# Performance work log

Hardware: AMD Instinct MI355X
Metric: run time of the kernel (lower is better)

Reference implementation:

```python
import jax, jax.numpy as jnp
import numpy as np

DIM = 1024
NUM_HEADS = 16
HEAD_DIM = DIM // NUM_HEADS
EPS = 1e-6


def setup_inputs() -> dict:
    key = jax.random.key(0)
    ks = jax.random.split(key, 9)
    B, S = 4, 4096
    std = 1.0 / np.sqrt(DIM)
    inp = {
        "x": jax.random.normal(ks[0], (B, S, DIM), dtype=jnp.float32),
        "attention_mask": jnp.ones((B, S), dtype=jnp.float32),
        "Wq": jax.random.normal(ks[1], (DIM, DIM), dtype=jnp.float32) * std,
        "bq": jnp.zeros((DIM,), dtype=jnp.float32),
        "Wk": jax.random.normal(ks[2], (DIM, DIM), dtype=jnp.float32) * std,
        "bk": jnp.zeros((DIM,), dtype=jnp.float32),
        "Wv": jax.random.normal(ks[3], (DIM, DIM), dtype=jnp.float32) * std,
        "bv": jnp.zeros((DIM,), dtype=jnp.float32),
        "Wo": jax.random.normal(ks[4], (DIM, DIM), dtype=jnp.float32) * std,
        "bo": jnp.zeros((DIM,), dtype=jnp.float32),
    }
    return inp


def _phi(x):
    # ELU + 1 feature map (positive-valued kernel features)
    return jax.nn.elu(x) + 1.0


def reference(x, attention_mask, Wq, bq, Wk, bk, Wv, bv, Wo, bo):
    B, S, _ = x.shape
    H, D = NUM_HEADS, HEAD_DIM
    q = (x @ Wq.T + bq).reshape(B, S, H, D)
    k = (x @ Wk.T + bk).reshape(B, S, H, D)
    v = (x @ Wv.T + bv).reshape(B, S, H, D)
    q = _phi(q)
    k = _phi(k)
    m = attention_mask[:, :, None, None]
    k = k * m
    v = v * m
    # kv state: [B, H, D, D]
    kv = jnp.einsum("bshd,bshm->bhdm", k, v)
    qkv = jnp.einsum("bshd,bhdm->bshm", q, kv)
    k_sum = k.sum(axis=1)  # [B, H, D]
    normalizer = jnp.einsum("bshd,bhd->bsh", q, k_sum) + EPS
    out = (qkv / normalizer[..., None]).reshape(B, S, DIM)
    return out @ Wo.T + bo
```

## Files before the change

kernel.cpp:

```cpp
#include <hip/hip_runtime.h>

typedef unsigned short u16;
typedef float f32x4 __attribute__((ext_vector_type(4)));
typedef __bf16 bf16x8 __attribute__((ext_vector_type(8)));
typedef unsigned short us8 __attribute__((ext_vector_type(8)));
typedef __attribute__((address_space(3))) const char* lds3_t;

#define EPS_ 1e-6f

__device__ __forceinline__ u16 f2bf(float f) {
    unsigned u = __float_as_uint(f);
    u += 0x7FFFu + ((u >> 16) & 1u);
    return (u16)(u >> 16);
}
__device__ __forceinline__ float bf2f(u16 h) {
    return __uint_as_float(((unsigned)h) << 16);
}
__device__ __forceinline__ void gload_lds16(const void* g, void* l) {
    __builtin_amdgcn_global_load_lds(
        (const __attribute__((address_space(1))) void*)g,
        (__attribute__((address_space(3))) void*)l, 16, 0, 0);
}

__global__ __launch_bounds__(256) void f32_to_bf16_kernel(
    const float* __restrict__ src, u16* __restrict__ dst, int n4)
{
    int i = blockIdx.x * 256 + threadIdx.x;
    if (i >= n4) return;
    float4 f = ((const float4*)src)[i];
    ushort4 o;
    o.x = f2bf(f.x); o.y = f2bf(f.y); o.z = f2bf(f.z); o.w = f2bf(f.w);
    ((ushort4*)dst)[i] = o;
}

__global__ __launch_bounds__(256) void w_convert_fused(
    const float* __restrict__ Wq, const float* __restrict__ Wk,
    const float* __restrict__ Wv, const float* __restrict__ bq,
    const float* __restrict__ bk, const float* __restrict__ bv,
    u16* __restrict__ wqkvbf, float* __restrict__ bcat)
{
    int b = blockIdx.x;
    if (b < 3072) {
        const float* src = (b < 1024) ? Wq : ((b < 2048) ? Wk : Wv);
        int which = b >> 10, lb = b & 1023;
        int i = lb * 256 + threadIdx.x;
        float4 f = ((const float4*)src)[i];
        ushort4 o;
        o.x = f2bf(f.x); o.y = f2bf(f.y); o.z = f2bf(f.z); o.w = f2bf(f.w);
        ((ushort4*)(wqkvbf + (size_t)which * 1048576))[i] = o;
    } else {
        int which = b - 3072;
        const float* src = (which == 0) ? bq : ((which == 1) ? bk : bv);
        ((float4*)(bcat + which * 1024))[threadIdx.x] =
            ((const float4*)src)[threadIdx.x];
    }
}


__device__ __forceinline__ void stage_half(
    const u16* __restrict__ src, int K, int kbase, char* slot, int tid)
{
    const int w = tid >> 6, l = tid & 63;
    #pragma unroll
    for (int j = 0; j < 2; ++j) {
        int c16 = j * 512 + w * 64 + l;
        int row = c16 >> 2;
        int sl  = c16 & 3;
        int ksrc = kbase + ((sl ^ ((row >> 1) & 3)) << 3);
        gload_lds16(src + (size_t)row * K + ksrc, slot + j * 8192 + w * 1024);
    }
}

#define BARRIER()  asm volatile("s_barrier" ::: "memory")
#define VMCNT4()   asm volatile("s_waitcnt vmcnt(4)" ::: "memory")
#define VMCNT0()   asm volatile("s_waitcnt vmcnt(0)" ::: "memory")

#define DSR_(dst_, base_, OFFSTR_) \
    asm volatile("ds_read_b128 %0, %1 offset:" OFFSTR_ \
                 : "=v"(dst_) : "v"((lds3_t)(base_)))
#define DSR(dst_, base_, OFF_) DSR_(dst_, base_, #OFF_)

#define LGKM_(NSTR_) asm volatile("s_waitcnt lgkmcnt(" NSTR_ ")" ::: "memory")
#define LGKM(N_) do { LGKM_(#N_); __builtin_amdgcn_sched_barrier(0); } while (0)

#define MFMA1(M_, N_, AF_, BF_) \
    acc[M_][N_] = __builtin_amdgcn_mfma_f32_16x16x32_bf16(BF_, AF_, acc[M_][N_], 0, 0, 0)

#define QUAD(M0, A0_, A1_, A2_, A3_, B0_, B1_, B2_, B3_) do { \
    __builtin_amdgcn_s_setprio(1); \
    MFMA1(M0+0, 0, A0_, B0_); MFMA1(M0+0, 1, A0_, B1_); MFMA1(M0+0, 2, A0_, B2_); MFMA1(M0+0, 3, A0_, B3_); \
    MFMA1(M0+1, 0, A1_, B0_); MFMA1(M0+1, 1, A1_, B1_); MFMA1(M0+1, 2, A1_, B2_); MFMA1(M0+1, 3, A1_, B3_); \
    MFMA1(M0+2, 0, A2_, B0_); MFMA1(M0+2, 1, A2_, B1_); MFMA1(M0+2, 2, A2_, B2_); MFMA1(M0+2, 3, A2_, B3_); \
    MFMA1(M0+3, 0, A3_, B0_); MFMA1(M0+3, 1, A3_, B1_); MFMA1(M0+3, 2, A3_, B2_); MFMA1(M0+3, 3, A3_, B3_); \
    __builtin_amdgcn_s_setprio(0); \
} while (0)

template<int MODE>
__global__ __launch_bounds__(512, 2) void gemm8p(
    const u16* __restrict__ A, const u16* __restrict__ B,
    const float* __restrict__ bias,
    u16* __restrict__ oq, u16* __restrict__ ok, u16* __restrict__ ov,
    float* __restrict__ outf, int M, int N, int K)
{
    extern __shared__ char lds[];
    const int tid  = threadIdx.x;
    const int lane = tid & 63;
    const int wv   = tid >> 6;
    const int wm   = wv >> 2;
    const int wn   = wv & 3;
    const int NT = K >> 6;

    int bx, by;
    {
        const int gx = gridDim.x;
        int wg  = blockIdx.y * gx + blockIdx.x;
        int cpx = (gx * gridDim.y) >> 3;
        int swz = (wg & 7) * cpx + (wg >> 3);
        bx = swz % gx; by = swz / gx;
    }

    const u16* Ab = A + (size_t)by * 256 * K;
    const u16* Bb = B + (size_t)bx * 256 * K;

    const int i  = lane & 15, g = lane >> 4;
    const int fo = ((g ^ ((i >> 1) & 3)) << 4);
    const int aoff = (wm * 128 + i) * 64 + fo;
    const int boff = (wn * 64 + i) * 64 + fo;

    f32x4 acc[8][4];
    #pragma unroll
    for (int m = 0; m < 8; ++m)
        #pragma unroll
        for (int n = 0; n < 4; ++n) {
            acc[m][n][0] = 0.f; acc[m][n][1] = 0.f;
            acc[m][n][2] = 0.f; acc[m][n][3] = 0.f;
        }

    stage_half(Ab, K, 0,  lds + 0,             tid);
    stage_half(Bb, K, 0,  lds + 16384,         tid);
    stage_half(Ab, K, 32, lds + 32768,         tid);
    stage_half(Bb, K, 32, lds + 49152,         tid);
    stage_half(Ab, K, 64, lds + 65536 + 0,     tid);
    stage_half(Bb, K, 64, lds + 65536 + 16384, tid);

    for (int t = 0; t < NT; ++t) {
        char* cb = lds + ((t & 1) << 16);
        char* nb = lds + (((t + 1) & 1) << 16);
        const int t1 = (t + 1 < NT) ? t + 1 : NT - 1;
        const int t2 = (t + 2 < NT) ? t + 2 : NT - 1;

        VMCNT4();
        BARRIER();

        const char* aK0 = cb + aoff;
        const char* bK0 = cb + 16384 + boff;
        const char* aK1 = cb + 32768 + aoff;
        const char* bK1 = cb + 49152 + boff;

        bf16x8 aL0, aL1, aL2, aL3, aH0, aH1, aH2, aH3, b00, b01, b02, b03;
        bf16x8 cL0, cL1, cL2, cL3, cH0, cH1, cH2, cH3, b10, b11, b12, b13;

        DSR(b00, bK0, 0); DSR(b01, bK0, 1024); DSR(b02, bK0, 2048); DSR(b03, bK0, 3072);
        DSR(aL0, aK0, 0); DSR(aL1, aK0, 1024); DSR(aL2, aK0, 2048); DSR(aL3, aK0, 3072);
        DSR(aH0, aK0, 4096); DSR(aH1, aK0, 5120); DSR(aH2, aK0, 6144); DSR(aH3, aK0, 7168);

        stage_half(Ab, K, t1 * 64 + 32, nb + 32768, tid);
        stage_half(Bb, K, t1 * 64 + 32, nb + 49152, tid);

        LGKM(4);
        QUAD(0, aL0, aL1, aL2, aL3, b00, b01, b02, b03);

        DSR(b10, bK1, 0); DSR(b11, bK1, 1024); DSR(b12, bK1, 2048); DSR(b13, bK1, 3072);
        DSR(cL0, aK1, 0); DSR(cL1, aK1, 1024); DSR(cL2, aK1, 2048); DSR(cL3, aK1, 3072);
        DSR(cH0, aK1, 4096); DSR(cH1, aK1, 5120); DSR(cH2, aK1, 6144); DSR(cH3, aK1, 7168);

        LGKM(12);
        QUAD(4, aH0, aH1, aH2, aH3, b00, b01, b02, b03);

        BARRIER();
        stage_half(Ab, K, t2 * 64, cb + 0,     tid);
        stage_half(Bb, K, t2 * 64, cb + 16384, tid);

        LGKM(4);
        QUAD(0, cL0, cL1, cL2, cL3, b10, b11, b12, b13);
        LGKM(0);
        QUAD(4, cH0, cH1, cH2, cH3, b10, b11, b12, b13);
    }
    VMCNT0();

    const int rowg0 = by * 256 + wm * 128;
    const int colg0 = bx * 256 + wn * 64;

    if (MODE == 1) {
        const int which = colg0 >> 10;
        u16* dst = (which == 0) ? oq : ((which == 1) ? ok : ov);
        const bool dophi = (which < 2);
        const int cbo = colg0 & 1023;
        float4 bs[4];
        #pragma unroll
        for (int n = 0; n < 4; ++n)
            bs[n] = *(const float4*)(bias + colg0 + n * 16 + g * 4);
        #pragma unroll
        for (int m = 0; m < 8; ++m) {
            int row = rowg0 + m * 16 + i;
            #pragma unroll
            for (int n = 0; n < 4; ++n) {
                float v0 = acc[m][n][0] + bs[n].x;
                float v1 = acc[m][n][1] + bs[n].y;
                float v2 = acc[m][n][2] + bs[n].z;
                float v3 = acc[m][n][3] + bs[n].w;
                if (dophi) {
                    v0 = (v0 > 0.f) ? (v0 + 1.f) : __expf(v0);
                    v1 = (v1 > 0.f) ? (v1 + 1.f) : __expf(v1);
                    v2 = (v2 > 0.f) ? (v2 + 1.f) : __expf(v2);
                    v3 = (v3 > 0.f) ? (v3 + 1.f) : __expf(v3);
                }
                ushort4 o;
                o.x = f2bf(v0); o.y = f2bf(v1); o.z = f2bf(v2); o.w = f2bf(v3);
                *(ushort4*)(dst + (size_t)row * 1024 + cbo + n * 16 + g * 4) = o;
            }
        }
    } else {
        float4 bs[4];
        #pragma unroll
        for (int n = 0; n < 4; ++n)
            bs[n] = *(const float4*)(bias + colg0 + n * 16 + g * 4);
        #pragma unroll
        for (int m = 0; m < 8; ++m) {
            int row = rowg0 + m * 16 + i;
            #pragma unroll
            for (int n = 0; n < 4; ++n) {
                float4 o;
                o.x = acc[m][n][0] + bs[n].x;
                o.y = acc[m][n][1] + bs[n].y;
                o.z = acc[m][n][2] + bs[n].z;
                o.w = acc[m][n][3] + bs[n].w;
                *(float4*)(outf + (size_t)row * N + colg0 + n * 16 + g * 4) = o;
            }
        }
    }
}

__global__ __launch_bounds__(256) void kv_partial(
    const u16* __restrict__ kbf, const u16* __restrict__ vbf,
    const float* __restrict__ mask, float* __restrict__ kvp, float* __restrict__ ksp)
{
    const int bh = blockIdx.x, ch = blockIdx.y;
    const int b = bh >> 4, h = bh & 15;
    const int tid = threadIdx.x;
    __shared__ __align__(16) float ks[32][64];
    __shared__ __align__(16) float vs[32][64];
    const int dg = tid >> 4, mg = tid & 15;
    float acc[4][4] = {};
    float ksa[4] = {};
    const int s0 = ch * 256;
    const int lr = tid >> 3, lc = (tid & 7) * 8;
    for (int sb = 0; sb < 256; sb += 32) {
        {
            size_t grow = (size_t)b * 4096 + (s0 + sb + lr);
            float mm = mask[grow];
            size_t off = (grow << 10) + (h << 6) + lc;
            us8 ku = __builtin_bit_cast(us8, *(const bf16x8*)(kbf + off));
            us8 vu = __builtin_bit_cast(us8, *(const bf16x8*)(vbf + off));
            float4 k0, k1, v0, v1;
            k0.x = bf2f(ku[0]) * mm; k0.y = bf2f(ku[1]) * mm;
            k0.z = bf2f(ku[2]) * mm; k0.w = bf2f(ku[3]) * mm;
            k1.x = bf2f(ku[4]) * mm; k1.y = bf2f(ku[5]) * mm;
            k1.z = bf2f(ku[6]) * mm; k1.w = bf2f(ku[7]) * mm;
            v0.x = bf2f(vu[0]) * mm; v0.y = bf2f(vu[1]) * mm;
            v0.z = bf2f(vu[2]) * mm; v0.w = bf2f(vu[3]) * mm;
            v1.x = bf2f(vu[4]) * mm; v1.y = bf2f(vu[5]) * mm;
            v1.z = bf2f(vu[6]) * mm; v1.w = bf2f(vu[7]) * mm;
            *(float4*)&ks[lr][lc]     = k0;
            *(float4*)&ks[lr][lc + 4] = k1;
            *(float4*)&vs[lr][lc]     = v0;
            *(float4*)&vs[lr][lc + 4] = v1;
        }
        __syncthreads();
        #pragma unroll
        for (int ss = 0; ss < 32; ++ss) {
            float4 k4 = *(const float4*)&ks[ss][dg << 2];
            float4 v4 = *(const float4*)&vs[ss][mg << 2];
            float ka[4] = {k4.x, k4.y, k4.z, k4.w};
            float va[4] = {v4.x, v4.y, v4.z, v4.w};
            #pragma unroll
            for (int di = 0; di < 4; ++di) {
                ksa[di] += ka[di];
                #pragma unroll
                for (int mi = 0; mi < 4; ++mi) acc[di][mi] += ka[di] * va[mi];
            }
        }
        __syncthreads();
    }
    float* o = kvp + (((size_t)ch * 64 + bh) << 12);
    #pragma unroll
    for (int di = 0; di < 4; ++di)
        #pragma unroll
        for (int mi = 0; mi < 4; ++mi)
            o[(dg * 4 + di) * 64 + (mg * 4 + mi)] = acc[di][mi];
    if (mg == 0) {
        float* os = ksp + (((size_t)ch * 64 + bh) << 6);
        #pragma unroll
        for (int di = 0; di < 4; ++di) os[dg * 4 + di] = ksa[di];
    }
}

__global__ __launch_bounds__(256) void kv_reduce(
    const float* __restrict__ kvp, const float* __restrict__ ksp,
    u16* __restrict__ kvTbf, u16* __restrict__ ksumbf)
{
    const int bh = blockIdx.x, tid = threadIdx.x;
    for (int idx = tid; idx < 4096; idx += 256) {
        float s = 0.f;
        #pragma unroll
        for (int c = 0; c < 16; ++c) s += kvp[(((size_t)c * 64 + bh) << 12) + idx];
        int d = idx >> 6, m = idx & 63;
        kvTbf[((size_t)bh << 12) + (m << 6) + d] = f2bf(s);
    }
    if (tid < 64) {
        float s = 0.f;
        #pragma unroll
        for (int c = 0; c < 16; ++c) s += ksp[(((size_t)c * 64 + bh) << 6) + tid];
        ksumbf[(bh << 6) + tid] = f2bf(s);
    }
}

__global__ __launch_bounds__(256) void attn_kernel(
    const u16* __restrict__ qbf, const u16* __restrict__ kvTbf,
    const u16* __restrict__ ksumbf, u16* __restrict__ attnbf)
{
    const int bh = blockIdx.x;
    const int b = bh >> 4, h = bh & 15;
    const int tid = threadIdx.x, lane = tid & 63, wv = tid >> 6;
    __shared__ __align__(16) u16 kvs[64 * 64];
    __shared__ __align__(16) u16 kss[64];

    {
        const uint4* src = (const uint4*)(kvTbf + ((size_t)bh << 12));
        for (int u = tid; u < 512; u += 256) {
            uint4 d4 = src[u];
            int m = u >> 3, slot = u & 7;
            *(uint4*)((char*)kvs + m * 128 + ((slot ^ (m & 7)) << 4)) = d4;
        }
        if (tid < 32)
            ((unsigned*)kss)[tid] = ((const unsigned*)(ksumbf + ((size_t)bh << 6)))[tid];
    }
    __syncthreads();

    bf16x8 bfr[2][4], bnf[2];
    #pragma unroll
    for (int kk = 0; kk < 2; ++kk) {
        int kslot = kk * 4 + (lane >> 4);
        #pragma unroll
        for (int n = 0; n < 4; ++n) {
            int m = n * 16 + (lane & 15);
            bfr[kk][n] = *(const bf16x8*)((const char*)kvs + m * 128 +
                                          ((kslot ^ (m & 7)) << 4));
        }
        #pragma unroll
        for (int i2 = 0; i2 < 8; ++i2) bnf[kk][i2] = (__bf16)0.0f;
        if ((lane & 15) == 0)
            bnf[kk] = *(const bf16x8*)((const char*)kss + (kslot << 4));
    }

    const int sbase = blockIdx.y * 256 + wv * 16;
    for (int it = 0; it < 4; ++it) {
        const int st = sbase + it * 64;
        f32x4 acc[4], nacc;
        #pragma unroll
        for (int n = 0; n < 4; ++n) {
            acc[n][0] = 0.f; acc[n][1] = 0.f; acc[n][2] = 0.f; acc[n][3] = 0.f;
        }
        nacc[0] = 0.f; nacc[1] = 0.f; nacc[2] = 0.f; nacc[3] = 0.f;
        #pragma unroll
        for (int kk = 0; kk < 2; ++kk) {
            size_t goff = (((size_t)(b * 4096 + st + (lane & 15))) << 10) +
                          (h << 6) + kk * 32 + ((lane >> 4) << 3);
            bf16x8 af = *(const bf16x8*)(qbf + goff);
            #pragma unroll
            for (int n = 0; n < 4; ++n)
                acc[n] = __builtin_amdgcn_mfma_f32_16x16x32_bf16(af, bfr[kk][n], acc[n], 0, 0, 0);
            nacc = __builtin_amdgcn_mfma_f32_16x16x32_bf16(af, bnf[kk], nacc, 0, 0, 0);
        }
        float inv[4];
        #pragma unroll
        for (int j = 0; j < 4; ++j) {
            float nj = __shfl(nacc[j], lane & 48);
            inv[j] = 1.0f / (nj + EPS_);
        }
        #pragma unroll
        for (int n = 0; n < 4; ++n)
            #pragma unroll
            for (int j = 0; j < 4; ++j) {
                int row = st + ((lane >> 4) << 2) + j;
                attnbf[(((size_t)(b * 4096 + row)) << 10) + (h << 6) + n * 16 + (lane & 15)]
                    = f2bf(acc[n][j] * inv[j]);
            }
    }
}

extern "C" void kernel_launch(void* const* d_in, const int* in_sizes, int n_in,
                              void* d_out, int out_size, void* d_ws, size_t ws_size,
                              hipStream_t stream) {
    const float* x    = (const float*)d_in[0];
    const float* mask = (const float*)d_in[1];
    const float* Wq   = (const float*)d_in[2];
    const float* bq   = (const float*)d_in[3];
    const float* Wk   = (const float*)d_in[4];
    const float* bk   = (const float*)d_in[5];
    const float* Wv   = (const float*)d_in[6];
    const float* bv   = (const float*)d_in[7];
    const float* Wo   = (const float*)d_in[8];
    const float* bo   = (const float*)d_in[9];
    float* out = (float*)d_out;

    if (ws_size < 142606336u) return;

    char* ws = (char*)d_ws;
    u16*   xbf    = (u16*)ws;
    u16*   wqkvbf = (u16*)(ws + 33554432);
    float* bcat   = (float*)(ws + 39845888);
    u16*   qbf    = (u16*)(ws + 41943040);
    u16*   kbf    = qbf + 16777216;
    u16*   vbf    = kbf + 16777216;
    u16*   attnbf = kbf;
    float* kvp    = (float*)ws;
    float* ksp    = (float*)(ws + 16777216);
    u16*   kvTbf  = (u16*)(ws + 17039360);
    u16*   ksumbf = (u16*)(ws + 17563648);
    u16*   wobf   = (u16*)(ws + 20971520);

    f32_to_bf16_kernel<<<16384, 256, 0, stream>>>(x, xbf, 16777216 / 4);
    w_convert_fused<<<3075, 256, 0, stream>>>(Wq, Wk, Wv, bq, bk, bv, wqkvbf, bcat);

    gemm8p<1><<<dim3(12, 64), 512, 131072, stream>>>(
        xbf, wqkvbf, bcat, qbf, kbf, vbf, nullptr, 16384, 3072, 1024);

    f32_to_bf16_kernel<<<1024, 256, 0, stream>>>(Wo, wobf, 1048576 / 4);

    kv_partial<<<dim3(64, 16), 256, 0, stream>>>(kbf, vbf, mask, kvp, ksp);
    kv_reduce<<<64, 256, 0, stream>>>(kvp, ksp, kvTbf, ksumbf);

    attn_kernel<<<dim3(64, 16), 256, 0, stream>>>(qbf, kvTbf, ksumbf, attnbf);

    gemm8p<0><<<dim3(4, 64), 512, 131072, stream>>>(
        attnbf, wobf, bo, nullptr, nullptr, nullptr, out, 16384, 1024, 1024);
}
```

Baseline: 225.4 us.

## Shrink GEMM block tile to 256x128 with 4 waves and triple-buffered K32 pipeline

```diff
diff --git a/kernel.cpp b/kernel.cpp
--- a/kernel.cpp
+++ b/kernel.cpp
@@ -57,22 +57,35 @@
 }
 
 
-__device__ __forceinline__ void stage_half(
+__device__ __forceinline__ void stage_a(
+    const u16* __restrict__ src, int K, int kbase, char* slot, int tid)
+{
+    const int w = tid >> 6, l = tid & 63;
+    #pragma unroll
+    for (int j = 0; j < 4; ++j) {
+        int c16 = j * 256 + w * 64 + l;
+        int row = c16 >> 2;
+        int sl  = c16 & 3;
+        int ksrc = kbase + ((sl ^ ((row >> 1) & 3)) << 3);
+        gload_lds16(src + (size_t)row * K + ksrc, slot + j * 4096 + w * 1024);
+    }
+}
+__device__ __forceinline__ void stage_b(
     const u16* __restrict__ src, int K, int kbase, char* slot, int tid)
 {
     const int w = tid >> 6, l = tid & 63;
     #pragma unroll
     for (int j = 0; j < 2; ++j) {
-        int c16 = j * 512 + w * 64 + l;
+        int c16 = j * 256 + w * 64 + l;
         int row = c16 >> 2;
         int sl  = c16 & 3;
         int ksrc = kbase + ((sl ^ ((row >> 1) & 3)) << 3);
-        gload_lds16(src + (size_t)row * K + ksrc, slot + j * 8192 + w * 1024);
+        gload_lds16(src + (size_t)row * K + ksrc, slot + j * 4096 + w * 1024);
     }
 }
 
 #define BARRIER()  asm volatile("s_barrier" ::: "memory")
-#define VMCNT4()   asm volatile("s_waitcnt vmcnt(4)" ::: "memory")
+#define VMCNT6()   asm volatile("s_waitcnt vmcnt(6)" ::: "memory")
 #define VMCNT0()   asm volatile("s_waitcnt vmcnt(0)" ::: "memory")
 
 #define DSR_(dst_, base_, OFFSTR_) \
@@ -96,7 +109,7 @@
 } while (0)
 
 template<int MODE>
-__global__ __launch_bounds__(512, 2) void gemm8p(
+__global__ __launch_bounds__(256, 2) void gemm8p(
     const u16* __restrict__ A, const u16* __restrict__ B,
     const float* __restrict__ bias,
     u16* __restrict__ oq, u16* __restrict__ ok, u16* __restrict__ ov,
@@ -106,9 +119,9 @@
     const int tid  = threadIdx.x;
     const int lane = tid & 63;
     const int wv   = tid >> 6;
-    const int wm   = wv >> 2;
-    const int wn   = wv & 3;
-    const int NT = K >> 6;
+    const int wm   = wv >> 1;
+    const int wn   = wv & 1;
+    const int NT = K >> 5;
 
     int bx, by;
     {
@@ -120,7 +133,7 @@
     }
 
     const u16* Ab = A + (size_t)by * 256 * K;
-    const u16* Bb = B + (size_t)bx * 256 * K;
+    const u16* Bb = B + (size_t)bx * 128 * K;
 
     const int i  = lane & 15, g = lane >> 4;
     const int fo = ((g ^ ((i >> 1) & 3)) << 4);
@@ -136,60 +149,39 @@
             acc[m][n][2] = 0.f; acc[m][n][3] = 0.f;
         }
 
-    stage_half(Ab, K, 0,  lds + 0,             tid);
-    stage_half(Bb, K, 0,  lds + 16384,         tid);
-    stage_half(Ab, K, 32, lds + 32768,         tid);
-    stage_half(Bb, K, 32, lds + 49152,         tid);
-    stage_half(Ab, K, 64, lds + 65536 + 0,     tid);
-    stage_half(Bb, K, 64, lds + 65536 + 16384, tid);
+    stage_a(Ab, K, 0,  lds + 0,             tid);
+    stage_b(Bb, K, 0,  lds + 16384,         tid);
+    stage_a(Ab, K, 32, lds + 24576,         tid);
+    stage_b(Bb, K, 32, lds + 24576 + 16384, tid);
 
     for (int t = 0; t < NT; ++t) {
-        char* cb = lds + ((t & 1) << 16);
-        char* nb = lds + (((t + 1) & 1) << 16);
-        const int t1 = (t + 1 < NT) ? t + 1 : NT - 1;
+        char* cb = lds + (t % 3) * 24576;
+        char* sb = lds + ((t + 2) % 3) * 24576;
         const int t2 = (t + 2 < NT) ? t + 2 : NT - 1;
 
-        VMCNT4();
+        VMCNT6();
         BARRIER();
 
-        const char* aK0 = cb + aoff;
-        const char* bK0 = cb + 16384 + boff;
-        const char* aK1 = cb + 32768 + aoff;
-        const char* bK1 = cb + 49152 + boff;
-
-        bf16x8 aL0, aL1, aL2, aL3, aH0, aH1, aH2, aH3, b00, b01, b02, b03;
-        bf16x8 cL0, cL1, cL2, cL3, cH0, cH1, cH2, cH3, b10, b11, b12, b13;
-
-        DSR(b00, bK0, 0); DSR(b01, bK0, 1024); DSR(b02, bK0, 2048); DSR(b03, bK0, 3072);
-        DSR(aL0, aK0, 0); DSR(aL1, aK0, 1024); DSR(aL2, aK0, 2048); DSR(aL3, aK0, 3072);
-        DSR(aH0, aK0, 4096); DSR(aH1, aK0, 5120); DSR(aH2, aK0, 6144); DSR(aH3, aK0, 7168);
-
-        stage_half(Ab, K, t1 * 64 + 32, nb + 32768, tid);
-        stage_half(Bb, K, t1 * 64 + 32, nb + 49152, tid);
+        stage_a(Ab, K, t2 * 32, sb,         tid);
+        stage_b(Bb, K, t2 * 32, sb + 16384, tid);
+
+        const char* aB = cb + aoff;
+        const char* bB = cb + 16384 + boff;
+        bf16x8 a0, a1, a2, a3, a4, a5, a6, a7, b0, b1, b2, b3;
+
+        DSR(b0, bB, 0); DSR(b1, bB, 1024); DSR(b2, bB, 2048); DSR(b3, bB, 3072);
+        DSR(a0, aB, 0); DSR(a1, aB, 1024); DSR(a2, aB, 2048); DSR(a3, aB, 3072);
+        DSR(a4, aB, 4096); DSR(a5, aB, 5120); DSR(a6, aB, 6144); DSR(a7, aB, 7168);
 
         LGKM(4);
-        QUAD(0, aL0, aL1, aL2, aL3, b00, b01, b02, b03);
-
-        DSR(b10, bK1, 0); DSR(b11, bK1, 1024); DSR(b12, bK1, 2048); DSR(b13, bK1, 3072);
-        DSR(cL0, aK1, 0); DSR(cL1, aK1, 1024); DSR(cL2, aK1, 2048); DSR(cL3, aK1, 3072);
-        DSR(cH0, aK1, 4096); DSR(cH1, aK1, 5120); DSR(cH2, aK1, 6144); DSR(cH3, aK1, 7168);
-
-        LGKM(12);
-        QUAD(4, aH0, aH1, aH2, aH3, b00, b01, b02, b03);
-
-        BARRIER();
-        stage_half(Ab, K, t2 * 64, cb + 0,     tid);
-        stage_half(Bb, K, t2 * 64, cb + 16384, tid);
-
-        LGKM(4);
-        QUAD(0, cL0, cL1, cL2, cL3, b10, b11, b12, b13);
+        QUAD(0, a0, a1, a2, a3, b0, b1, b2, b3);
         LGKM(0);
-        QUAD(4, cH0, cH1, cH2, cH3, b10, b11, b12, b13);
+        QUAD(4, a4, a5, a6, a7, b0, b1, b2, b3);
     }
     VMCNT0();
 
     const int rowg0 = by * 256 + wm * 128;
-    const int colg0 = bx * 256 + wn * 64;
+    const int colg0 = bx * 128 + wn * 64;
 
     if (MODE == 1) {
         const int which = colg0 >> 10;
@@ -433,7 +425,7 @@
     f32_to_bf16_kernel<<<16384, 256, 0, stream>>>(x, xbf, 16777216 / 4);
     w_convert_fused<<<3075, 256, 0, stream>>>(Wq, Wk, Wv, bq, bk, bv, wqkvbf, bcat);
 
-    gemm8p<1><<<dim3(12, 64), 512, 131072, stream>>>(
+    gemm8p<1><<<dim3(24, 64), 256, 73728, stream>>>(
         xbf, wqkvbf, bcat, qbf, kbf, vbf, nullptr, 16384, 3072, 1024);
 
     f32_to_bf16_kernel<<<1024, 256, 0, stream>>>(Wo, wobf, 1048576 / 4);
@@ -443,6 +435,6 @@
 
     attn_kernel<<<dim3(64, 16), 256, 0, stream>>>(qbf, kvTbf, ksumbf, attnbf);
 
-    gemm8p<0><<<dim3(4, 64), 512, 131072, stream>>>(
+    gemm8p<0><<<dim3(8, 64), 256, 73728, stream>>>(
         attnbf, wobf, bo, nullptr, nullptr, nullptr, out, 16384, 1024, 1024);
 }
```

Result: slower. 240.3 us (+6.6%).
